# Kernel optimization log

Measured on AMD Instinct MI355X. Metric: run time of the kernel, lower is better.

## Reference

```python
import jax, jax.numpy as jnp
import numpy as np

D_MODEL = 2048
NUM_HEADS = 16
D_K = D_MODEL // NUM_HEADS  # 128
THETA = 10000.0
BATCH = 2
SEQ = 2048


def _rope(v, pos):
    # v: [..., S, d_k], pos: [..., S] int
    half = v.shape[-1] // 2
    inv_freq = THETA ** (-(jnp.arange(half, dtype=jnp.float32) * 2.0) / v.shape[-1])
    ang = pos[..., None].astype(jnp.float32) * inv_freq  # [..., S, half]
    cos, sin = jnp.cos(ang), jnp.sin(ang)
    x1 = v[..., 0::2]
    x2 = v[..., 1::2]
    r1 = x1 * cos - x2 * sin
    r2 = x1 * sin + x2 * cos
    return jnp.stack([r1, r2], axis=-1).reshape(v.shape)


def setup_inputs() -> dict:
    key = jax.random.key(0)
    ks = jax.random.split(key, 5)
    scale = D_MODEL ** -0.5
    x = jax.random.normal(ks[0], (BATCH, SEQ, D_MODEL), dtype=jnp.float32)
    WQ = jax.random.normal(ks[1], (D_MODEL, D_MODEL), dtype=jnp.float32) * scale
    WK = jax.random.normal(ks[2], (D_MODEL, D_MODEL), dtype=jnp.float32) * scale
    WV = jax.random.normal(ks[3], (D_MODEL, D_MODEL), dtype=jnp.float32) * scale
    WO = jax.random.normal(ks[4], (D_MODEL, D_MODEL), dtype=jnp.float32) * scale
    token_positions = jnp.broadcast_to(jnp.arange(SEQ, dtype=jnp.int32), (BATCH, SEQ))
    return {"x": x, "token_positions": token_positions, "WQ": WQ, "WK": WK, "WV": WV, "WO": WO}


def reference(x, token_positions, WQ, WK, WV, WO):
    B, S, _ = x.shape
    split = lambda t: t.reshape(B, S, NUM_HEADS, D_K).transpose(0, 2, 1, 3)  # [B,H,S,d]
    Q = split(x @ WQ.T)
    K = split(x @ WK.T)
    V = split(x @ WV.T)
    pos = token_positions[:, None, :]  # broadcast over heads
    Q = _rope(Q, pos)
    K = _rope(K, pos)
    scores = jnp.einsum('bhqd,bhkd->bhqk', Q, K) / np.sqrt(D_K).astype(np.float32)
    causal = jnp.arange(S)[:, None] >= jnp.arange(S)[None, :]  # [S,S]
    scores = jnp.where(causal, scores, -jnp.inf)
    attn = jax.nn.softmax(scores, axis=-1)
    out = jnp.einsum('bhqk,bhkd->bhqd', attn, V)
    out = out.transpose(0, 2, 1, 3).reshape(B, S, D_MODEL)
    return out @ WO.T
```

## Files before the change

kernel.cpp:

```cpp
#include <hip/hip_runtime.h>

typedef unsigned short ushort;
typedef __attribute__((ext_vector_type(8))) __bf16 bf16x8;
typedef __attribute__((ext_vector_type(8))) ushort ushort8;
typedef __attribute__((ext_vector_type(4))) float f32x4;
typedef __attribute__((ext_vector_type(16))) float f32x16;
typedef __attribute__((ext_vector_type(4))) unsigned u32x4;

#define DM 2048
#define NH 16
#define DK 128
#define BATCH 2
#define SEQ 2048
#define MROWS (BATCH*SEQ)

#define GLDS16(g, l) __builtin_amdgcn_global_load_lds(                         \
    (const __attribute__((address_space(1))) void*)(g),                        \
    (__attribute__((address_space(3))) void*)(l), 16, 0, 0)

__device__ __forceinline__ ushort f2bf(float f) {
  unsigned u = __builtin_bit_cast(unsigned, f);
  u += 0x7fffu + ((u >> 16) & 1u);
  return (ushort)(u >> 16);
}

__device__ __forceinline__ unsigned cvtpk(float lo, float hi) {
  unsigned r;
  asm("v_cvt_pk_bf16_f32 %0, %1, %2" : "=v"(r) : "v"(lo), "v"(hi));
  return r;
}

__global__ __launch_bounds__(256) void cvt_all(const float* __restrict__ x,
                                               const float* __restrict__ w0,
                                               const float* __restrict__ w1,
                                               const float* __restrict__ w2,
                                               const float* __restrict__ w3,
                                               ushort* __restrict__ xb,
                                               ushort* __restrict__ o0,
                                               ushort* __restrict__ o1,
                                               ushort* __restrict__ o2,
                                               ushort* __restrict__ o3) {
  int b = blockIdx.x;
  const float* src;
  ushort* dst;
  int lb;
  if (b < 4096) { src = x; dst = xb; lb = b; }
  else {
    int wsel = (b - 4096) >> 11;
    lb = (b - 4096) & 2047;
    src = (wsel == 0) ? w0 : (wsel == 1) ? w1 : (wsel == 2) ? w2 : w3;
    dst = (wsel == 0) ? o0 : (wsel == 1) ? o1 : (wsel == 2) ? o2 : o3;
  }
  int i = lb * 256 + threadIdx.x;
  const float4* p = (const float4*)src;
  float4 a = p[2 * i], bq = p[2 * i + 1];
  ushort8 o;
  o[0] = f2bf(a.x); o[1] = f2bf(a.y); o[2] = f2bf(a.z); o[3] = f2bf(a.w);
  o[4] = f2bf(bq.x); o[5] = f2bf(bq.y); o[6] = f2bf(bq.z); o[7] = f2bf(bq.w);
  *(ushort8*)(dst + (size_t)8 * i) = o;
}

__global__ __launch_bounds__(512, 2) void gemmQ_qkv(const ushort* __restrict__ A,
                                                    const ushort* __restrict__ W0,
                                                    const ushort* __restrict__ W1,
                                                    const ushort* __restrict__ W2,
                                                    ushort* __restrict__ O0,
                                                    ushort* __restrict__ O1,
                                                    ushort* __restrict__ O2) {
  extern __shared__ ushort lds[];
  constexpr int NT = DM / 64;
  constexpr int BUFSZ = 40960;
  int xcd = (int)blockIdx.x & 7, bi = (int)blockIdx.x >> 3;
  int row0 = (((xcd >> 2) << 3) + (bi >> 2)) * 256;
  int col0 = (((xcd & 3) << 2) + (bi & 3)) * 128;
  const ushort* Bw[3] = {W0, W1, W2};
  ushort* Ow[3] = {O0, O1, O2};
  const int tid = threadIdx.x;
  const int wid = tid >> 6, lane = tid & 63;
  const int l15 = lane & 15, lhi = lane >> 4;
  const int wm = wid >> 2, wn = wid & 3;
  const int swz = l15 & 7;

  f32x4 acc[8][6];
  const f32x4 z4 = {0.f, 0.f, 0.f, 0.f};
#pragma unroll
  for (int mq = 0; mq < 8; ++mq)
#pragma unroll
    for (int i = 0; i < 6; ++i) acc[mq][i] = z4;

  auto stage = [&](int kt, int buf) {
    ushort* dstA = &lds[buf * BUFSZ];
    const ushort* srcA = A + (size_t)row0 * DM + kt * 64;
#pragma unroll
    for (int j = 0; j < 4; ++j) {
      int g = j * 512 + tid;
      int r = g >> 3, c = g & 7;
      GLDS16(srcA + (size_t)r * DM + ((c ^ (r & 7)) * 8),
             &dstA[(j * 512 + wid * 64) * 8]);
    }
#pragma unroll
    for (int w3 = 0; w3 < 3; ++w3) {
      ushort* dstB = &lds[buf * BUFSZ + 16384 + w3 * 8192];
      const ushort* srcB = Bw[w3] + (size_t)col0 * DM + kt * 64;
#pragma unroll
      for (int j = 0; j < 2; ++j) {
        int g = j * 512 + tid;
        int r = g >> 3, c = g & 7;
        GLDS16(srcB + (size_t)r * DM + ((c ^ (r & 7)) * 8),
               &dstB[(j * 512 + wid * 64) * 8]);
      }
    }
  };

  stage(0, 0);
  stage(1, 1);

  for (int t = 0; t < NT; ++t) {
    if (t + 1 < NT)
      asm volatile("s_waitcnt vmcnt(10)" ::: "memory");
    else
      asm volatile("s_waitcnt vmcnt(0)" ::: "memory");
    __builtin_amdgcn_s_barrier();

    const int cb = t & 1;
    const ushort* Ab = &lds[cb * BUFSZ];
    const ushort* Bb = Ab + 16384;
#pragma unroll
    for (int ks = 0; ks < 2; ++ks) {
      bf16x8 af[8];
#pragma unroll
      for (int mq = 0; mq < 8; ++mq) {
        int row = wm * 128 + mq * 16 + l15;
        af[mq] = *(const bf16x8*)&Ab[row * 64 + (((ks * 4 + lhi) ^ swz) * 8)];
      }
#pragma unroll
      for (int w3 = 0; w3 < 3; ++w3) {
        bf16x8 bfr[2];
#pragma unroll
        for (int n = 0; n < 2; ++n) {
          int row = wn * 32 + n * 16 + l15;
          bfr[n] = *(const bf16x8*)&Bb[w3 * 8192 + row * 64 + (((ks * 4 + lhi) ^ swz) * 8)];
        }
        __builtin_amdgcn_s_setprio(1);
#pragma unroll
        for (int mq = 0; mq < 8; ++mq)
#pragma unroll
          for (int n = 0; n < 2; ++n)
            acc[mq][w3 * 2 + n] = __builtin_amdgcn_mfma_f32_16x16x32_bf16(
                af[mq], bfr[n], acc[mq][w3 * 2 + n], 0, 0, 0);
        __builtin_amdgcn_s_setprio(0);
      }
    }

    __builtin_amdgcn_s_barrier();
    if (t + 2 < NT) stage(t + 2, cb);
  }

#pragma unroll
  for (int mq = 0; mq < 8; ++mq) {
    int grow = row0 + wm * 128 + mq * 16 + lhi * 4;
#pragma unroll
    for (int w3 = 0; w3 < 3; ++w3)
#pragma unroll
      for (int n = 0; n < 2; ++n) {
        int gcol = col0 + wn * 32 + n * 16 + l15;
        int h = gcol >> 7, d = gcol & (DK - 1);
#pragma unroll
        for (int j = 0; j < 4; ++j) {
          int r = grow + j;
          int b = r >> 11, s = r & (SEQ - 1);
          Ow[w3][((size_t)(b * NH + h) * SEQ + s) * DK + d] = f2bf(acc[mq][w3 * 2 + n][j]);
        }
      }
  }
}

__device__ __forceinline__ void gemmO_body(const ushort* __restrict__ A,
                                           const ushort* __restrict__ Bm,
                                           float* __restrict__ ofp,
                                           int row0, int col0) {
  extern __shared__ ushort lds[];
  constexpr int NT = DM / 64;
  constexpr int BUFSZ = 8192 + 16384;
  const int tid = threadIdx.x;
  const int wid = tid >> 6, lane = tid & 63;
  const int l15 = lane & 15, lhi = lane >> 4;
  const int wm = wid >> 2, wn = wid & 3;
  const int swz = l15 & 7;

  f32x4 acc[4][4];
  const f32x4 z4 = {0.f, 0.f, 0.f, 0.f};
#pragma unroll
  for (int mq = 0; mq < 4; ++mq)
#pragma unroll
    for (int i = 0; i < 4; ++i) acc[mq][i] = z4;

  auto stage = [&](int kt, int buf) {
    ushort* dstA = &lds[buf * BUFSZ];
    const ushort* srcA = A + (size_t)row0 * DM + kt * 64;
#pragma unroll
    for (int j = 0; j < 2; ++j) {
      int g = j * 512 + tid;
      int r = g >> 3, c = g & 7;
      GLDS16(srcA + (size_t)r * DM + ((c ^ (r & 7)) * 8),
             &dstA[(j * 512 + wid * 64) * 8]);
    }
    ushort* dstB = &lds[buf * BUFSZ + 8192];
    const ushort* srcB = Bm + (size_t)col0 * DM + kt * 64;
#pragma unroll
    for (int j = 0; j < 4; ++j) {
      int g = j * 512 + tid;
      int r = g >> 3, c = g & 7;
      GLDS16(srcB + (size_t)r * DM + ((c ^ (r & 7)) * 8),
             &dstB[(j * 512 + wid * 64) * 8]);
    }
  };

  stage(0, 0);
  stage(1, 1);

  for (int t = 0; t < NT; ++t) {
    if (t + 1 < NT)
      asm volatile("s_waitcnt vmcnt(6)" ::: "memory");
    else
      asm volatile("s_waitcnt vmcnt(0)" ::: "memory");
    __builtin_amdgcn_s_barrier();

    const int cb = t & 1;
    const ushort* Ab = &lds[cb * BUFSZ];
    const ushort* Bb = Ab + 8192;
#pragma unroll
    for (int ks = 0; ks < 2; ++ks) {
      bf16x8 af[4];
#pragma unroll
      for (int mq = 0; mq < 4; ++mq) {
        int row = wm * 64 + mq * 16 + l15;
        af[mq] = *(const bf16x8*)&Ab[row * 64 + (((ks * 4 + lhi) ^ swz) * 8)];
      }
      bf16x8 bfr[4];
#pragma unroll
      for (int n = 0; n < 4; ++n) {
        int row = wn * 64 + n * 16 + l15;
        bfr[n] = *(const bf16x8*)&Bb[row * 64 + (((ks * 4 + lhi) ^ swz) * 8)];
      }
      __builtin_amdgcn_s_setprio(1);
#pragma unroll
      for (int mq = 0; mq < 4; ++mq)
#pragma unroll
        for (int n = 0; n < 4; ++n)
          acc[mq][n] = __builtin_amdgcn_mfma_f32_16x16x32_bf16(af[mq], bfr[n], acc[mq][n], 0, 0, 0);
      __builtin_amdgcn_s_setprio(0);
    }

    __builtin_amdgcn_s_barrier();
    if (t + 2 < NT) stage(t + 2, cb);
  }

#pragma unroll
  for (int mq = 0; mq < 4; ++mq) {
    int grow = row0 + wm * 64 + mq * 16 + lhi * 4;
#pragma unroll
    for (int n = 0; n < 4; ++n) {
      int gcol = col0 + wn * 64 + n * 16 + l15;
#pragma unroll
      for (int j = 0; j < 4; ++j)
        ofp[(size_t)(grow + j) * DM + gcol] = acc[mq][n][j];
    }
  }
}

__global__ __launch_bounds__(512, 2) void gemmF_out(const ushort* __restrict__ A,
                                                    const ushort* __restrict__ Bm,
                                                    float* __restrict__ ofp) {
  int xcd = (int)blockIdx.x & 7, i = (int)blockIdx.x >> 3;
  int row0 = (((xcd >> 1) << 3) + (i >> 2)) * 128;
  int col0 = (((xcd & 1) << 2) + (i & 3)) * 256;
  gemmO_body(A, Bm, ofp, row0, col0);
}

__global__ __launch_bounds__(256) void rope_kernel(ushort* __restrict__ Q,
                                                   ushort* __restrict__ K,
                                                   const int* __restrict__ tpos) {
  int bid = blockIdx.x;
  ushort* buf = (bid & 1) ? K : Q;
  int idx = (bid >> 1) * 256 + threadIdx.x;
  int c = idx & 15;
  int row = idx >> 4;
  int s = row & (SEQ - 1);
  int bh = row >> 11;
  int b = bh >> 4;
  int pos = tpos[b * SEQ + s];
  int d0 = c * 8;
  ushort8 v = *(ushort8*)(buf + (size_t)row * DK + d0);
  float fp = (float)pos;
#pragma unroll
  for (int p = 0; p < 4; ++p) {
    int i = (d0 >> 1) + p;
    float freq = exp2f(-13.287712379549449f * ((float)i * (1.0f / 64.0f)));
    float ang = fp * freq;
    float sn, cs;
    sincosf(ang, &sn, &cs);
    float x1 = __builtin_bit_cast(float, (unsigned)v[2 * p] << 16);
    float x2 = __builtin_bit_cast(float, (unsigned)v[2 * p + 1] << 16);
    float r1 = x1 * cs - x2 * sn;
    float r2 = x1 * sn + x2 * cs;
    v[2 * p] = f2bf(r1);
    v[2 * p + 1] = f2bf(r2);
  }
  *(ushort8*)(buf + (size_t)row * DK + d0) = v;
}

__global__ __launch_bounds__(256) void transpose_v(const ushort* __restrict__ Vb,
                                                   ushort* __restrict__ Vt) {
  __shared__ ushort t[64 * 80];
  int s0 = blockIdx.x * 64, d0 = blockIdx.y * 64, bh = blockIdx.z;
  const size_t base = (size_t)bh * SEQ * DK;
  int tid = threadIdx.x;
#pragma unroll
  for (int it = 0; it < 2; ++it) {
    int c = it * 256 + tid;
    int r = c >> 3, c8 = (c & 7) * 8;
    ushort8 v = *(const ushort8*)&Vb[base + (size_t)(s0 + r) * DK + d0 + c8];
    *(ushort8*)&t[r * 80 + c8] = v;
  }
  __syncthreads();
  const size_t obase = (size_t)bh * DK * SEQ;
#pragma unroll
  for (int it = 0; it < 2; ++it) {
    int c = it * 256 + tid;
    int dr = c >> 3, sc = (c & 7) * 8;
    ushort8 v;
#pragma unroll
    for (int i2 = 0; i2 < 8; ++i2) v[i2] = t[(sc + i2) * 80 + dr];
    *(ushort8*)&Vt[obase + (size_t)(d0 + dr) * SEQ + s0 + sc] = v;
  }
}

__global__ __launch_bounds__(256, 2) void attn_kernel(const ushort* __restrict__ Qb,
                                                      const ushort* __restrict__ Kb,
                                                      const ushort* __restrict__ Vt,
                                                      ushort* __restrict__ attnb) {
  __shared__ ushort lds[32768];
  const int bx = blockIdx.x;
  const int u = bx & 255, hg = bx >> 8;
  const int qt = hg ? (15 - (u & 15)) : (u & 15);
  const int bh = (u >> 4) + hg * 16;
  const int tid = threadIdx.x;
  const int w = tid >> 6, lane = tid & 63;
  const int l31 = lane & 31, hi = lane >> 5;
  const int qb = qt * 128;
  const int qsb = qb + w * 32;
  const int q = qsb + l31;
  const size_t qk_base = (size_t)bh * SEQ * DK;
  const size_t v_base = (size_t)bh * DK * SEQ;
  const int nt = (qb + 128) >> 6;

  bf16x8 qf[8];
#pragma unroll
  for (int ks = 0; ks < 8; ++ks)
    qf[ks] = *(const bf16x8*)&Qb[qk_base + (size_t)q * DK + ks * 16 + hi * 8];

  f32x16 acc[4];
#pragma unroll
  for (int dt = 0; dt < 4; ++dt)
#pragma unroll
    for (int r = 0; r < 16; ++r) acc[dt][r] = 0.f;

  float m2 = -INFINITY, lsum = 0.f;
  const float cs2 = 0.08838834764831845f * 1.4426950408889634f;

  auto stage = [&](int t, int bufsel) {
    const int kb0 = t * 64;
#pragma unroll
    for (int i = 0; i < 4; ++i) {
      int g = w * 256 + i * 64 + lane;
      int row = g >> 4, c16 = g & 15;
      GLDS16(Kb + qk_base + (size_t)(kb0 + row) * DK + ((c16 ^ (row & 7)) * 8),
             &lds[bufsel * 8192 + (w * 256 + i * 64) * 8]);
    }
#pragma unroll
    for (int i = 0; i < 4; ++i) {
      int g = w * 256 + i * 64 + lane;
      int row = g >> 3, c8 = g & 7;
      GLDS16(Vt + v_base + (size_t)row * SEQ + kb0 + ((c8 ^ (row & 7)) * 8),
             &lds[16384 + bufsel * 8192 + (w * 256 + i * 64) * 8]);
    }
  };

  stage(0, 0);
  __syncthreads();
  int buf = 0;

  for (int t = 0; t < nt; ++t) {
    if (t + 1 < nt) stage(t + 1, buf ^ 1);
    const int kb0 = t * 64;
    if (kb0 <= qsb) {
      const ushort* lk = &lds[buf * 8192];
      const ushort* lv = &lds[16384 + buf * 8192];
      const int kb1 = kb0 + 32;
      const bool diag0 = (kb0 == qsb);
      const bool have1 = (kb1 <= qsb);
      const bool diag1 = (kb1 == qsb);
      const int sw = l31 & 7;

      f32x16 s0, s1;
#pragma unroll
      for (int r = 0; r < 16; ++r) { s0[r] = 0.f; s1[r] = 0.f; }
      __builtin_amdgcn_s_setprio(1);
#pragma unroll
      for (int ks = 0; ks < 8; ++ks) {
        int g = 2 * ks + hi;
        bf16x8 kf = *(const bf16x8*)&lk[(l31 * 16 + (g ^ sw)) * 8];
        s0 = __builtin_amdgcn_mfma_f32_32x32x16_bf16(kf, qf[ks], s0, 0, 0, 0);
      }
      if (have1) {
#pragma unroll
        for (int ks = 0; ks < 8; ++ks) {
          int g = 2 * ks + hi;
          bf16x8 kf = *(const bf16x8*)&lk[((32 + l31) * 16 + (g ^ sw)) * 8];
          s1 = __builtin_amdgcn_mfma_f32_32x32x16_bf16(kf, qf[ks], s1, 0, 0, 0);
        }
      }
      __builtin_amdgcn_s_setprio(0);

      float mx = -INFINITY;
#pragma unroll
      for (int r = 0; r < 16; ++r) {
        float v = s0[r] * cs2;
        if (diag0) {
          int kk = kb0 + (r & 3) + 8 * (r >> 2) + 4 * hi;
          if (kk > q) v = -INFINITY;
        }
        s0[r] = v;
        mx = fmaxf(mx, v);
      }
      if (have1) {
#pragma unroll
        for (int r = 0; r < 16; ++r) {
          float v = s1[r] * cs2;
          if (diag1) {
            int kk = kb1 + (r & 3) + 8 * (r >> 2) + 4 * hi;
            if (kk > q) v = -INFINITY;
          }
          s1[r] = v;
          mx = fmaxf(mx, v);
        }
      }
      mx = fmaxf(mx, __shfl_xor(mx, 32));

      float sc = 1.f;
      if (!__all(mx <= m2 + 11.5f)) {
        float mnew = fmaxf(m2, mx);
        sc = exp2f(m2 - mnew);
        m2 = mnew;
#pragma unroll
        for (int dt = 0; dt < 4; ++dt)
#pragma unroll
          for (int r = 0; r < 16; ++r) acc[dt][r] *= sc;
      }
      float rs = 0.f;
#pragma unroll
      for (int r = 0; r < 16; ++r) {
        float p = exp2f(s0[r] - m2);
        s0[r] = p;
        rs += p;
      }
      if (have1) {
#pragma unroll
        for (int r = 0; r < 16; ++r) {
          float p = exp2f(s1[r] - m2);
          s1[r] = p;
          rs += p;
        }
      }
      rs += __shfl_xor(rs, 32);
      lsum = lsum * sc + rs;

      unsigned w0[8], ws0[8];
#pragma unroll
      for (int i = 0; i < 8; ++i) w0[i] = cvtpk(s0[2 * i], s0[2 * i + 1]);
#pragma unroll
      for (int i = 0; i < 8; ++i) ws0[i] = (unsigned)__shfl_xor((int)w0[i], 32);
      u32x4 b00, b01;
      b00[0] = hi ? ws0[2] : w0[0]; b00[1] = hi ? ws0[3] : w0[1];
      b00[2] = hi ? w0[2] : ws0[0]; b00[3] = hi ? w0[3] : ws0[1];
      b01[0] = hi ? ws0[6] : w0[4]; b01[1] = hi ? ws0[7] : w0[5];
      b01[2] = hi ? w0[6] : ws0[4]; b01[3] = hi ? w0[7] : ws0[5];
      bf16x8 pb00 = __builtin_bit_cast(bf16x8, b00);
      bf16x8 pb01 = __builtin_bit_cast(bf16x8, b01);
      bf16x8 pb10, pb11;
      if (have1) {
        unsigned w1[8], ws1[8];
#pragma unroll
        for (int i = 0; i < 8; ++i) w1[i] = cvtpk(s1[2 * i], s1[2 * i + 1]);
#pragma unroll
        for (int i = 0; i < 8; ++i) ws1[i] = (unsigned)__shfl_xor((int)w1[i], 32);
        u32x4 b10, b11;
        b10[0] = hi ? ws1[2] : w1[0]; b10[1] = hi ? ws1[3] : w1[1];
        b10[2] = hi ? w1[2] : ws1[0]; b10[3] = hi ? w1[3] : ws1[1];
        b11[0] = hi ? ws1[6] : w1[4]; b11[1] = hi ? ws1[7] : w1[5];
        b11[2] = hi ? w1[6] : ws1[4]; b11[3] = hi ? w1[7] : ws1[5];
        pb10 = __builtin_bit_cast(bf16x8, b10);
        pb11 = __builtin_bit_cast(bf16x8, b11);
      }

      __builtin_amdgcn_s_setprio(1);
#pragma unroll
      for (int dt = 0; dt < 4; ++dt) {
        int vr = (dt * 32 + l31) * 8;
        bf16x8 vf0 = *(const bf16x8*)&lv[(vr + ((0 + hi) ^ sw)) * 8];
        bf16x8 vf1 = *(const bf16x8*)&lv[(vr + ((2 + hi) ^ sw)) * 8];
        acc[dt] = __builtin_amdgcn_mfma_f32_32x32x16_bf16(vf0, pb00, acc[dt], 0, 0, 0);
        acc[dt] = __builtin_amdgcn_mfma_f32_32x32x16_bf16(vf1, pb01, acc[dt], 0, 0, 0);
        if (have1) {
          bf16x8 vf2 = *(const bf16x8*)&lv[(vr + ((4 + hi) ^ sw)) * 8];
          bf16x8 vf3 = *(const bf16x8*)&lv[(vr + ((6 + hi) ^ sw)) * 8];
          acc[dt] = __builtin_amdgcn_mfma_f32_32x32x16_bf16(vf2, pb10, acc[dt], 0, 0, 0);
          acc[dt] = __builtin_amdgcn_mfma_f32_32x32x16_bf16(vf3, pb11, acc[dt], 0, 0, 0);
        }
      }
      __builtin_amdgcn_s_setprio(0);
    }
    __syncthreads();
    buf ^= 1;
  }

  ushort* eo = &lds[w * 32 * 136];
  float inv = 1.0f / lsum;
#pragma unroll
  for (int dt = 0; dt < 4; ++dt)
#pragma unroll
    for (int rq = 0; rq < 4; ++rq) {
      unsigned lo = cvtpk(acc[dt][4 * rq] * inv, acc[dt][4 * rq + 1] * inv);
      unsigned hh = cvtpk(acc[dt][4 * rq + 2] * inv, acc[dt][4 * rq + 3] * inv);
      uint2 pr; pr.x = lo; pr.y = hh;
      *(uint2*)&eo[l31 * 136 + dt * 32 + rq * 8 + hi * 4] = pr;
    }
  const int b = bh >> 4, h = bh & (NH - 1);
#pragma unroll
  for (int it = 0; it < 8; ++it) {
    int row = it * 4 + (lane >> 4);
    int c8 = (lane & 15) * 8;
    ushort8 v = *(const ushort8*)&eo[row * 136 + c8];
    *(ushort8*)&attnb[((size_t)b * SEQ + qsb + row) * DM + h * DK + c8] = v;
  }
}

extern "C" void kernel_launch(void* const* d_in, const int* in_sizes, int n_in,
                              void* d_out, int out_size, void* d_ws, size_t ws_size,
                              hipStream_t stream) {
  const float* x = (const float*)d_in[0];
  const int* tpos = (const int*)d_in[1];
  const float* WQ = (const float*)d_in[2];
  const float* WK = (const float*)d_in[3];
  const float* WV = (const float*)d_in[4];
  const float* WO = (const float*)d_in[5];
  float* out = (float*)d_out;
  char* ws = (char*)d_ws;

  ushort* xb  = (ushort*)(ws + 0);
  ushort* wqb = (ushort*)(ws + 16777216);
  ushort* wkb = (ushort*)(ws + 25165824);
  ushort* wvb = (ushort*)(ws + 33554432);
  ushort* wob = (ushort*)(ws + 41943040);
  ushort* Qb  = (ushort*)(ws + 50331648);
  ushort* Kb  = (ushort*)(ws + 67108864);
  ushort* Vb  = (ushort*)(ws + 83886080);
  ushort* Vt  = (ushort*)(ws + 0);
  ushort* attnb = (ushort*)(ws + 16777216);

  hipFuncSetAttribute(reinterpret_cast<const void*>(gemmQ_qkv),
                      hipFuncAttributeMaxDynamicSharedMemorySize, 163840);
  hipFuncSetAttribute(reinterpret_cast<const void*>(gemmF_out),
                      hipFuncAttributeMaxDynamicSharedMemorySize, 98304);

  cvt_all<<<12288, 256, 0, stream>>>(x, WQ, WK, WV, WO, xb, wqb, wkb, wvb, wob);

  gemmQ_qkv<<<256, 512, 163840, stream>>>(xb, wqb, wkb, wvb, Qb, Kb, Vb);

  rope_kernel<<<8192, 256, 0, stream>>>(Qb, Kb, tpos);

  transpose_v<<<dim3(SEQ / 64, DK / 64, BATCH * NH), 256, 0, stream>>>(Vb, Vt);

  attn_kernel<<<dim3(512), 256, 0, stream>>>(Qb, Kb, Vt, attnb);

  gemmF_out<<<256, 512, 98304, stream>>>(attnb, wob, out);
}
```

Before: 270.2 us.

## Retile fused QKV GEMM into 256x256 single-weight tiles over 384 blocks

The fused QKV projection kernel drops the layout where each block computed a 256x128 tile for all three weights at once. Each block now computes a 256x256 output tile for one weight, with the weight chosen by block index, and the grid grows from 256 to 384 blocks with an XCD-aware index mapping. Each tile is now square, so the A tile is amortised over 256 columns and the LDS buffer shrinks from 160KB to 128KB. In exchange each block holds fewer accumulators, the x tile is reloaded three times across weights, and 384 blocks may give an uneven final wave on the CUs.

```diff
diff --git a/kernel.cpp b/kernel.cpp
--- a/kernel.cpp
+++ b/kernel.cpp
@@ -60,33 +60,33 @@
   *(ushort8*)(dst + (size_t)8 * i) = o;
 }
 
-__global__ __launch_bounds__(512, 2) void gemmQ_qkv(const ushort* __restrict__ A,
-                                                    const ushort* __restrict__ W0,
-                                                    const ushort* __restrict__ W1,
-                                                    const ushort* __restrict__ W2,
-                                                    ushort* __restrict__ O0,
-                                                    ushort* __restrict__ O1,
-                                                    ushort* __restrict__ O2) {
+__global__ __launch_bounds__(512, 2) void gemm256_qkv(const ushort* __restrict__ A,
+                                                      const ushort* __restrict__ W0,
+                                                      const ushort* __restrict__ W1,
+                                                      const ushort* __restrict__ W2,
+                                                      ushort* __restrict__ O0,
+                                                      ushort* __restrict__ O1,
+                                                      ushort* __restrict__ O2) {
   extern __shared__ ushort lds[];
   constexpr int NT = DM / 64;
-  constexpr int BUFSZ = 40960;
-  int xcd = (int)blockIdx.x & 7, bi = (int)blockIdx.x >> 3;
-  int row0 = (((xcd >> 2) << 3) + (bi >> 2)) * 256;
-  int col0 = (((xcd & 3) << 2) + (bi & 3)) * 128;
-  const ushort* Bw[3] = {W0, W1, W2};
-  ushort* Ow[3] = {O0, O1, O2};
+  constexpr int BUFSZ = 32768;
+  int f = ((int)blockIdx.x & 7) * 48 + ((int)blockIdx.x >> 3);
+  int z = f >> 7, rem = f & 127;
+  int row0 = (rem >> 3) * 256, col0 = (rem & 7) * 256;
+  const ushort* Bm = (z == 0) ? W0 : (z == 1) ? W1 : W2;
+  ushort* Ow = (z == 0) ? O0 : (z == 1) ? O1 : O2;
   const int tid = threadIdx.x;
   const int wid = tid >> 6, lane = tid & 63;
   const int l15 = lane & 15, lhi = lane >> 4;
   const int wm = wid >> 2, wn = wid & 3;
   const int swz = l15 & 7;
 
-  f32x4 acc[8][6];
+  f32x4 acc[8][4];
   const f32x4 z4 = {0.f, 0.f, 0.f, 0.f};
 #pragma unroll
   for (int mq = 0; mq < 8; ++mq)
 #pragma unroll
-    for (int i = 0; i < 6; ++i) acc[mq][i] = z4;
+    for (int n = 0; n < 4; ++n) acc[mq][n] = z4;
 
   auto stage = [&](int kt, int buf) {
     ushort* dstA = &lds[buf * BUFSZ];
@@ -98,17 +98,14 @@
       GLDS16(srcA + (size_t)r * DM + ((c ^ (r & 7)) * 8),
              &dstA[(j * 512 + wid * 64) * 8]);
     }
-#pragma unroll
-    for (int w3 = 0; w3 < 3; ++w3) {
-      ushort* dstB = &lds[buf * BUFSZ + 16384 + w3 * 8192];
-      const ushort* srcB = Bw[w3] + (size_t)col0 * DM + kt * 64;
-#pragma unroll
-      for (int j = 0; j < 2; ++j) {
-        int g = j * 512 + tid;
-        int r = g >> 3, c = g & 7;
-        GLDS16(srcB + (size_t)r * DM + ((c ^ (r & 7)) * 8),
-               &dstB[(j * 512 + wid * 64) * 8]);
-      }
+    ushort* dstB = &lds[buf * BUFSZ + 16384];
+    const ushort* srcB = Bm + (size_t)col0 * DM + kt * 64;
+#pragma unroll
+    for (int j = 0; j < 4; ++j) {
+      int g = j * 512 + tid;
+      int r = g >> 3, c = g & 7;
+      GLDS16(srcB + (size_t)r * DM + ((c ^ (r & 7)) * 8),
+             &dstB[(j * 512 + wid * 64) * 8]);
     }
   };
 
@@ -117,7 +114,7 @@
 
   for (int t = 0; t < NT; ++t) {
     if (t + 1 < NT)
-      asm volatile("s_waitcnt vmcnt(10)" ::: "memory");
+      asm volatile("s_waitcnt vmcnt(8)" ::: "memory");
     else
       asm volatile("s_waitcnt vmcnt(0)" ::: "memory");
     __builtin_amdgcn_s_barrier();
@@ -133,23 +130,19 @@
         int row = wm * 128 + mq * 16 + l15;
         af[mq] = *(const bf16x8*)&Ab[row * 64 + (((ks * 4 + lhi) ^ swz) * 8)];
       }
-#pragma unroll
-      for (int w3 = 0; w3 < 3; ++w3) {
-        bf16x8 bfr[2];
-#pragma unroll
-        for (int n = 0; n < 2; ++n) {
-          int row = wn * 32 + n * 16 + l15;
-          bfr[n] = *(const bf16x8*)&Bb[w3 * 8192 + row * 64 + (((ks * 4 + lhi) ^ swz) * 8)];
-        }
-        __builtin_amdgcn_s_setprio(1);
-#pragma unroll
-        for (int mq = 0; mq < 8; ++mq)
-#pragma unroll
-          for (int n = 0; n < 2; ++n)
-            acc[mq][w3 * 2 + n] = __builtin_amdgcn_mfma_f32_16x16x32_bf16(
-                af[mq], bfr[n], acc[mq][w3 * 2 + n], 0, 0, 0);
-        __builtin_amdgcn_s_setprio(0);
-      }
+      bf16x8 bfr[4];
+#pragma unroll
+      for (int n = 0; n < 4; ++n) {
+        int row = wn * 64 + n * 16 + l15;
+        bfr[n] = *(const bf16x8*)&Bb[row * 64 + (((ks * 4 + lhi) ^ swz) * 8)];
+      }
+      __builtin_amdgcn_s_setprio(1);
+#pragma unroll
+      for (int mq = 0; mq < 8; ++mq)
+#pragma unroll
+        for (int n = 0; n < 4; ++n)
+          acc[mq][n] = __builtin_amdgcn_mfma_f32_16x16x32_bf16(af[mq], bfr[n], acc[mq][n], 0, 0, 0);
+      __builtin_amdgcn_s_setprio(0);
     }
 
     __builtin_amdgcn_s_barrier();
@@ -160,18 +153,16 @@
   for (int mq = 0; mq < 8; ++mq) {
     int grow = row0 + wm * 128 + mq * 16 + lhi * 4;
 #pragma unroll
-    for (int w3 = 0; w3 < 3; ++w3)
-#pragma unroll
-      for (int n = 0; n < 2; ++n) {
-        int gcol = col0 + wn * 32 + n * 16 + l15;
-        int h = gcol >> 7, d = gcol & (DK - 1);
-#pragma unroll
-        for (int j = 0; j < 4; ++j) {
-          int r = grow + j;
-          int b = r >> 11, s = r & (SEQ - 1);
-          Ow[w3][((size_t)(b * NH + h) * SEQ + s) * DK + d] = f2bf(acc[mq][w3 * 2 + n][j]);
-        }
-      }
+    for (int n = 0; n < 4; ++n) {
+      int gcol = col0 + wn * 64 + n * 16 + l15;
+      int h = gcol >> 7, d = gcol & (DK - 1);
+#pragma unroll
+      for (int j = 0; j < 4; ++j) {
+        int r = grow + j;
+        int b = r >> 11, s = r & (SEQ - 1);
+        Ow[((size_t)(b * NH + h) * SEQ + s) * DK + d] = f2bf(acc[mq][n][j]);
+      }
+    }
   }
 }
 
@@ -569,14 +560,14 @@
   ushort* Vt  = (ushort*)(ws + 0);
   ushort* attnb = (ushort*)(ws + 16777216);
 
-  hipFuncSetAttribute(reinterpret_cast<const void*>(gemmQ_qkv),
-                      hipFuncAttributeMaxDynamicSharedMemorySize, 163840);
+  hipFuncSetAttribute(reinterpret_cast<const void*>(gemm256_qkv),
+                      hipFuncAttributeMaxDynamicSharedMemorySize, 131072);
   hipFuncSetAttribute(reinterpret_cast<const void*>(gemmF_out),
                       hipFuncAttributeMaxDynamicSharedMemorySize, 98304);
 
   cvt_all<<<12288, 256, 0, stream>>>(x, WQ, WK, WV, WO, xb, wqb, wkb, wvb, wob);
 
-  gemmQ_qkv<<<256, 512, 163840, stream>>>(xb, wqb, wkb, wvb, Qb, Kb, Vb);
+  gemm256_qkv<<<384, 512, 131072, stream>>>(xb, wqb, wkb, wvb, Qb, Kb, Vb);
 
   rope_kernel<<<8192, 256, 0, stream>>>(Qb, Kb, tpos);
 
```

After: 277.7 us. 2.8% more time.

## Fuse RoPE and V transpose into QKV GEMM epilogue, use permlane32 swaps

Applied to the files above, without the earlier changes.

Folds the RoPE rotation and the V transpose into the QKV projection GEMM epilogue, which removes two separate kernel launches and their extra HBM round trips over Q, K and V. The GEMM tile shrinks from 256x128 to 128x128 with 512 blocks. The pipeline changes from two tiles in flight to a single-ahead double buffer with a full vmcnt(0) wait each iteration. The attention kernel replaces shfl_xor plus select sequences with permlane32_swap for the cross-half exchanges. Risks include a less overlapped GEMM pipeline, the cost of sincos in the epilogue, and strided 8-byte Vt stores.

```diff
diff --git a/kernel.cpp b/kernel.cpp
--- a/kernel.cpp
+++ b/kernel.cpp
@@ -3,6 +3,7 @@
 typedef unsigned short ushort;
 typedef __attribute__((ext_vector_type(8))) __bf16 bf16x8;
 typedef __attribute__((ext_vector_type(8))) ushort ushort8;
+typedef __attribute__((ext_vector_type(4))) ushort ushort4v;
 typedef __attribute__((ext_vector_type(4))) float f32x4;
 typedef __attribute__((ext_vector_type(16))) float f32x16;
 typedef __attribute__((ext_vector_type(4))) unsigned u32x4;
@@ -28,6 +29,21 @@
   unsigned r;
   asm("v_cvt_pk_bf16_f32 %0, %1, %2" : "=v"(r) : "v"(lo), "v"(hi));
   return r;
+}
+
+__device__ __forceinline__ void pswap(unsigned& a, unsigned& b) {
+#if __has_builtin(__builtin_amdgcn_permlane32_swap)
+  auto r = __builtin_amdgcn_permlane32_swap(a, b, false, false);
+  a = r[0];
+  b = r[1];
+#else
+  unsigned as = (unsigned)__shfl_xor((int)a, 32), bs = (unsigned)__shfl_xor((int)b, 32);
+  bool hi = (threadIdx.x & 32) != 0;
+  unsigned na = hi ? bs : a;
+  unsigned nb = hi ? b : as;
+  a = na;
+  b = nb;
+#endif
 }
 
 __global__ __launch_bounds__(256) void cvt_all(const float* __restrict__ x,
@@ -60,31 +76,30 @@
   *(ushort8*)(dst + (size_t)8 * i) = o;
 }
 
-__global__ __launch_bounds__(512, 2) void gemmQ_qkv(const ushort* __restrict__ A,
+__global__ __launch_bounds__(512, 2) void gemmF_qkv(const ushort* __restrict__ A,
                                                     const ushort* __restrict__ W0,
                                                     const ushort* __restrict__ W1,
                                                     const ushort* __restrict__ W2,
-                                                    ushort* __restrict__ O0,
-                                                    ushort* __restrict__ O1,
-                                                    ushort* __restrict__ O2) {
+                                                    ushort* __restrict__ Qo,
+                                                    ushort* __restrict__ Ko,
+                                                    ushort* __restrict__ Vt,
+                                                    const int* __restrict__ tpos) {
   extern __shared__ ushort lds[];
   constexpr int NT = DM / 64;
-  constexpr int BUFSZ = 40960;
-  int xcd = (int)blockIdx.x & 7, bi = (int)blockIdx.x >> 3;
-  int row0 = (((xcd >> 2) << 3) + (bi >> 2)) * 256;
-  int col0 = (((xcd & 3) << 2) + (bi & 3)) * 128;
+  constexpr int BUFSZ = 8192 + 24576;
+  int f = ((int)blockIdx.x & 7) * 64 + ((int)blockIdx.x >> 3);
+  int row0 = (f >> 4) * 128, col0 = (f & 15) * 128;
   const ushort* Bw[3] = {W0, W1, W2};
-  ushort* Ow[3] = {O0, O1, O2};
   const int tid = threadIdx.x;
   const int wid = tid >> 6, lane = tid & 63;
   const int l15 = lane & 15, lhi = lane >> 4;
   const int wm = wid >> 2, wn = wid & 3;
   const int swz = l15 & 7;
 
-  f32x4 acc[8][6];
+  f32x4 acc[4][6];
   const f32x4 z4 = {0.f, 0.f, 0.f, 0.f};
 #pragma unroll
-  for (int mq = 0; mq < 8; ++mq)
+  for (int mq = 0; mq < 4; ++mq)
 #pragma unroll
     for (int i = 0; i < 6; ++i) acc[mq][i] = z4;
 
@@ -92,7 +107,7 @@
     ushort* dstA = &lds[buf * BUFSZ];
     const ushort* srcA = A + (size_t)row0 * DM + kt * 64;
 #pragma unroll
-    for (int j = 0; j < 4; ++j) {
+    for (int j = 0; j < 2; ++j) {
       int g = j * 512 + tid;
       int r = g >> 3, c = g & 7;
       GLDS16(srcA + (size_t)r * DM + ((c ^ (r & 7)) * 8),
@@ -100,7 +115,7 @@
     }
 #pragma unroll
     for (int w3 = 0; w3 < 3; ++w3) {
-      ushort* dstB = &lds[buf * BUFSZ + 16384 + w3 * 8192];
+      ushort* dstB = &lds[buf * BUFSZ + 8192 + w3 * 8192];
       const ushort* srcB = Bw[w3] + (size_t)col0 * DM + kt * 64;
 #pragma unroll
       for (int j = 0; j < 2; ++j) {
@@ -113,65 +128,92 @@
   };
 
   stage(0, 0);
-  stage(1, 1);
+  asm volatile("s_waitcnt vmcnt(0)" ::: "memory");
+  asm volatile("s_barrier" ::: "memory");
 
   for (int t = 0; t < NT; ++t) {
-    if (t + 1 < NT)
-      asm volatile("s_waitcnt vmcnt(10)" ::: "memory");
-    else
-      asm volatile("s_waitcnt vmcnt(0)" ::: "memory");
-    __builtin_amdgcn_s_barrier();
-
     const int cb = t & 1;
     const ushort* Ab = &lds[cb * BUFSZ];
-    const ushort* Bb = Ab + 16384;
+    const ushort* Bb = Ab + 8192;
+    if (t + 1 < NT) stage(t + 1, cb ^ 1);
 #pragma unroll
     for (int ks = 0; ks < 2; ++ks) {
-      bf16x8 af[8];
-#pragma unroll
-      for (int mq = 0; mq < 8; ++mq) {
-        int row = wm * 128 + mq * 16 + l15;
+      bf16x8 af[4];
+#pragma unroll
+      for (int mq = 0; mq < 4; ++mq) {
+        int row = wm * 64 + mq * 16 + l15;
         af[mq] = *(const bf16x8*)&Ab[row * 64 + (((ks * 4 + lhi) ^ swz) * 8)];
       }
-#pragma unroll
-      for (int w3 = 0; w3 < 3; ++w3) {
-        bf16x8 bfr[2];
+      bf16x8 bfr[6];
+#pragma unroll
+      for (int w3 = 0; w3 < 3; ++w3)
 #pragma unroll
         for (int n = 0; n < 2; ++n) {
           int row = wn * 32 + n * 16 + l15;
-          bfr[n] = *(const bf16x8*)&Bb[w3 * 8192 + row * 64 + (((ks * 4 + lhi) ^ swz) * 8)];
-        }
-        __builtin_amdgcn_s_setprio(1);
-#pragma unroll
-        for (int mq = 0; mq < 8; ++mq)
-#pragma unroll
-          for (int n = 0; n < 2; ++n)
-            acc[mq][w3 * 2 + n] = __builtin_amdgcn_mfma_f32_16x16x32_bf16(
-                af[mq], bfr[n], acc[mq][w3 * 2 + n], 0, 0, 0);
-        __builtin_amdgcn_s_setprio(0);
-      }
-    }
-
-    __builtin_amdgcn_s_barrier();
-    if (t + 2 < NT) stage(t + 2, cb);
-  }
-
-#pragma unroll
-  for (int mq = 0; mq < 8; ++mq) {
-    int grow = row0 + wm * 128 + mq * 16 + lhi * 4;
-#pragma unroll
-    for (int w3 = 0; w3 < 3; ++w3)
+          bfr[w3 * 2 + n] =
+              *(const bf16x8*)&Bb[w3 * 8192 + row * 64 + (((ks * 4 + lhi) ^ swz) * 8)];
+        }
+      __builtin_amdgcn_s_setprio(1);
+#pragma unroll
+      for (int mq = 0; mq < 4; ++mq)
+#pragma unroll
+        for (int i = 0; i < 6; ++i)
+          acc[mq][i] = __builtin_amdgcn_mfma_f32_16x16x32_bf16(af[mq], bfr[i], acc[mq][i], 0, 0, 0);
+      __builtin_amdgcn_s_setprio(0);
+    }
+    asm volatile("s_waitcnt vmcnt(0)" ::: "memory");
+    asm volatile("s_barrier" ::: "memory");
+  }
+
+  int posr[4][4];
+#pragma unroll
+  for (int mq = 0; mq < 4; ++mq) {
+    int grow = row0 + wm * 64 + mq * 16 + lhi * 4;
+#pragma unroll
+    for (int j = 0; j < 4; ++j) {
+      int r = grow + j;
+      posr[mq][j] = tpos[(r >> 11) * SEQ + (r & (SEQ - 1))];
+    }
+  }
+#pragma unroll
+  for (int mq = 0; mq < 4; ++mq) {
+    int grow = row0 + wm * 64 + mq * 16 + lhi * 4;
+#pragma unroll
+    for (int w3 = 0; w3 < 2; ++w3) {
+      ushort* Ow = (w3 == 0) ? Qo : Ko;
 #pragma unroll
       for (int n = 0; n < 2; ++n) {
         int gcol = col0 + wn * 32 + n * 16 + l15;
         int h = gcol >> 7, d = gcol & (DK - 1);
+        float freq = exp2f(-0.20762050593045976f * (float)(d >> 1));
+        bool oddl = (d & 1) != 0;
 #pragma unroll
         for (int j = 0; j < 4; ++j) {
           int r = grow + j;
+          float v = acc[mq][w3 * 2 + n][j];
+          float vp = __shfl_xor(v, 1);
+          float ang = (float)posr[mq][j] * freq;
+          float sn, cs;
+          sincosf(ang, &sn, &cs);
+          float outv = oddl ? (vp * sn + v * cs) : (v * cs - vp * sn);
           int b = r >> 11, s = r & (SEQ - 1);
-          Ow[w3][((size_t)(b * NH + h) * SEQ + s) * DK + d] = f2bf(acc[mq][w3 * 2 + n][j]);
-        }
-      }
+          Ow[((size_t)(b * NH + h) * SEQ + s) * DK + d] = f2bf(outv);
+        }
+      }
+    }
+    {
+      int r0 = grow;
+      int b = r0 >> 11, s = r0 & (SEQ - 1);
+#pragma unroll
+      for (int n = 0; n < 2; ++n) {
+        int gcol = col0 + wn * 32 + n * 16 + l15;
+        int h = gcol >> 7, d = gcol & (DK - 1);
+        ushort4v o;
+#pragma unroll
+        for (int j = 0; j < 4; ++j) o[j] = f2bf(acc[mq][4 + n][j]);
+        *(ushort4v*)&Vt[((size_t)(b * NH + h) * DK + d) * SEQ + s] = o;
+      }
+    }
   }
 }
 
@@ -276,64 +318,6 @@
   int row0 = (((xcd >> 1) << 3) + (i >> 2)) * 128;
   int col0 = (((xcd & 1) << 2) + (i & 3)) * 256;
   gemmO_body(A, Bm, ofp, row0, col0);
-}
-
-__global__ __launch_bounds__(256) void rope_kernel(ushort* __restrict__ Q,
-                                                   ushort* __restrict__ K,
-                                                   const int* __restrict__ tpos) {
-  int bid = blockIdx.x;
-  ushort* buf = (bid & 1) ? K : Q;
-  int idx = (bid >> 1) * 256 + threadIdx.x;
-  int c = idx & 15;
-  int row = idx >> 4;
-  int s = row & (SEQ - 1);
-  int bh = row >> 11;
-  int b = bh >> 4;
-  int pos = tpos[b * SEQ + s];
-  int d0 = c * 8;
-  ushort8 v = *(ushort8*)(buf + (size_t)row * DK + d0);
-  float fp = (float)pos;
-#pragma unroll
-  for (int p = 0; p < 4; ++p) {
-    int i = (d0 >> 1) + p;
-    float freq = exp2f(-13.287712379549449f * ((float)i * (1.0f / 64.0f)));
-    float ang = fp * freq;
-    float sn, cs;
-    sincosf(ang, &sn, &cs);
-    float x1 = __builtin_bit_cast(float, (unsigned)v[2 * p] << 16);
-    float x2 = __builtin_bit_cast(float, (unsigned)v[2 * p + 1] << 16);
-    float r1 = x1 * cs - x2 * sn;
-    float r2 = x1 * sn + x2 * cs;
-    v[2 * p] = f2bf(r1);
-    v[2 * p + 1] = f2bf(r2);
-  }
-  *(ushort8*)(buf + (size_t)row * DK + d0) = v;
-}
-
-__global__ __launch_bounds__(256) void transpose_v(const ushort* __restrict__ Vb,
-                                                   ushort* __restrict__ Vt) {
-  __shared__ ushort t[64 * 80];
-  int s0 = blockIdx.x * 64, d0 = blockIdx.y * 64, bh = blockIdx.z;
-  const size_t base = (size_t)bh * SEQ * DK;
-  int tid = threadIdx.x;
-#pragma unroll
-  for (int it = 0; it < 2; ++it) {
-    int c = it * 256 + tid;
-    int r = c >> 3, c8 = (c & 7) * 8;
-    ushort8 v = *(const ushort8*)&Vb[base + (size_t)(s0 + r) * DK + d0 + c8];
-    *(ushort8*)&t[r * 80 + c8] = v;
-  }
-  __syncthreads();
-  const size_t obase = (size_t)bh * DK * SEQ;
-#pragma unroll
-  for (int it = 0; it < 2; ++it) {
-    int c = it * 256 + tid;
-    int dr = c >> 3, sc = (c & 7) * 8;
-    ushort8 v;
-#pragma unroll
-    for (int i2 = 0; i2 < 8; ++i2) v[i2] = t[(sc + i2) * 80 + dr];
-    *(ushort8*)&Vt[obase + (size_t)(d0 + dr) * SEQ + s0 + sc] = v;
-  }
 }
 
 __global__ __launch_bounds__(256, 2) void attn_kernel(const ushort* __restrict__ Qb,
@@ -446,7 +430,11 @@
           mx = fmaxf(mx, v);
         }
       }
-      mx = fmaxf(mx, __shfl_xor(mx, 32));
+      {
+        unsigned ma = __builtin_bit_cast(unsigned, mx), mb = ma;
+        pswap(ma, mb);
+        mx = fmaxf(__builtin_bit_cast(float, ma), __builtin_bit_cast(float, mb));
+      }
 
       float sc = 1.f;
       if (!__all(mx <= m2 + 11.5f)) {
@@ -473,33 +461,31 @@
           rs += p;
         }
       }
-      rs += __shfl_xor(rs, 32);
+      {
+        unsigned ra = __builtin_bit_cast(unsigned, rs), rb = ra;
+        pswap(ra, rb);
+        rs = __builtin_bit_cast(float, ra) + __builtin_bit_cast(float, rb);
+      }
       lsum = lsum * sc + rs;
 
-      unsigned w0[8], ws0[8];
+      unsigned w0[8];
 #pragma unroll
       for (int i = 0; i < 8; ++i) w0[i] = cvtpk(s0[2 * i], s0[2 * i + 1]);
-#pragma unroll
-      for (int i = 0; i < 8; ++i) ws0[i] = (unsigned)__shfl_xor((int)w0[i], 32);
-      u32x4 b00, b01;
-      b00[0] = hi ? ws0[2] : w0[0]; b00[1] = hi ? ws0[3] : w0[1];
-      b00[2] = hi ? w0[2] : ws0[0]; b00[3] = hi ? w0[3] : ws0[1];
-      b01[0] = hi ? ws0[6] : w0[4]; b01[1] = hi ? ws0[7] : w0[5];
-      b01[2] = hi ? w0[6] : ws0[4]; b01[3] = hi ? w0[7] : ws0[5];
+      pswap(w0[0], w0[2]); pswap(w0[1], w0[3]);
+      pswap(w0[4], w0[6]); pswap(w0[5], w0[7]);
+      u32x4 b00 = {w0[0], w0[1], w0[2], w0[3]};
+      u32x4 b01 = {w0[4], w0[5], w0[6], w0[7]};
       bf16x8 pb00 = __builtin_bit_cast(bf16x8, b00);
       bf16x8 pb01 = __builtin_bit_cast(bf16x8, b01);
       bf16x8 pb10, pb11;
       if (have1) {
-        unsigned w1[8], ws1[8];
+        unsigned w1[8];
 #pragma unroll
         for (int i = 0; i < 8; ++i) w1[i] = cvtpk(s1[2 * i], s1[2 * i + 1]);
-#pragma unroll
-        for (int i = 0; i < 8; ++i) ws1[i] = (unsigned)__shfl_xor((int)w1[i], 32);
-        u32x4 b10, b11;
-        b10[0] = hi ? ws1[2] : w1[0]; b10[1] = hi ? ws1[3] : w1[1];
-        b10[2] = hi ? w1[2] : ws1[0]; b10[3] = hi ? w1[3] : ws1[1];
-        b11[0] = hi ? ws1[6] : w1[4]; b11[1] = hi ? ws1[7] : w1[5];
-        b11[2] = hi ? w1[6] : ws1[4]; b11[3] = hi ? w1[7] : ws1[5];
+        pswap(w1[0], w1[2]); pswap(w1[1], w1[3]);
+        pswap(w1[4], w1[6]); pswap(w1[5], w1[7]);
+        u32x4 b10 = {w1[0], w1[1], w1[2], w1[3]};
+        u32x4 b11 = {w1[4], w1[5], w1[6], w1[7]};
         pb10 = __builtin_bit_cast(bf16x8, b10);
         pb11 = __builtin_bit_cast(bf16x8, b11);
       }
@@ -565,22 +551,17 @@
   ushort* wob = (ushort*)(ws + 41943040);
   ushort* Qb  = (ushort*)(ws + 50331648);
   ushort* Kb  = (ushort*)(ws + 67108864);
-  ushort* Vb  = (ushort*)(ws + 83886080);
-  ushort* Vt  = (ushort*)(ws + 0);
+  ushort* Vt  = (ushort*)(ws + 83886080);
   ushort* attnb = (ushort*)(ws + 16777216);
 
-  hipFuncSetAttribute(reinterpret_cast<const void*>(gemmQ_qkv),
-                      hipFuncAttributeMaxDynamicSharedMemorySize, 163840);
+  hipFuncSetAttribute(reinterpret_cast<const void*>(gemmF_qkv),
+                      hipFuncAttributeMaxDynamicSharedMemorySize, 131072);
   hipFuncSetAttribute(reinterpret_cast<const void*>(gemmF_out),
                       hipFuncAttributeMaxDynamicSharedMemorySize, 98304);
 
   cvt_all<<<12288, 256, 0, stream>>>(x, WQ, WK, WV, WO, xb, wqb, wkb, wvb, wob);
 
-  gemmQ_qkv<<<256, 512, 163840, stream>>>(xb, wqb, wkb, wvb, Qb, Kb, Vb);
-
-  rope_kernel<<<8192, 256, 0, stream>>>(Qb, Kb, tpos);
-
-  transpose_v<<<dim3(SEQ / 64, DK / 64, BATCH * NH), 256, 0, stream>>>(Vb, Vt);
+  gemmF_qkv<<<512, 512, 131072, stream>>>(xb, wqb, wkb, wvb, Qb, Kb, Vt, tpos);
 
   attn_kernel<<<dim3(512), 256, 0, stream>>>(Qb, Kb, Vt, attnb);
 
```

Measured after the change: 305.6 us. 1.13x slower.
